# Performance work log

Hardware: AMD Instinct MI355X
Metric: run time of the kernel (lower is better)

## Reference

```python
import jax, jax.numpy as jnp
import numpy as np

IN_FEATS = 512
OUT_FEATS = 512
N = 8192
M = 8192


def setup_inputs() -> dict:
    key = jax.random.key(0)
    k1, k2, k3 = jax.random.split(key, 3)
    feat_p = jax.random.normal(k1, (N, IN_FEATS), dtype=jnp.float32)
    feat_s = jax.random.normal(k2, (M, IN_FEATS), dtype=jnp.float32)
    # He (kaiming uniform) init: bound = sqrt(6 / fan_in)
    bound = float(np.sqrt(6.0 / IN_FEATS))
    weight_a = jax.random.uniform(k3, (IN_FEATS, OUT_FEATS), dtype=jnp.float32,
                                  minval=-bound, maxval=bound)
    return {"feat_p": feat_p, "feat_s": feat_s, "weight_a": weight_a}


def reference(feat_p, feat_s, weight_a):
    h_i = feat_p @ weight_a            # [N, out]
    h_j = feat_s @ weight_a            # [M, out]
    a_ij = jax.nn.relu(h_i @ h_j.T)    # [N, M]
    fro = jnp.sqrt(jnp.sum(a_ij * a_ij))
    alpha = a_ij / fro                 # global Frobenius-norm normalization
    c_i = alpha @ feat_s               # [N, in]
    return c_i
```

## Files before the change

kernel.cpp:

```cpp
#include <hip/hip_runtime.h>
#include <hip/hip_bf16.h>

#define NROWS 8192
#define DIM   512

typedef short v8s __attribute__((ext_vector_type(8)));
typedef short v4s __attribute__((ext_vector_type(4)));
typedef float v4f __attribute__((ext_vector_type(4)));

#define ASM_VMCNT(n) asm volatile("s_waitcnt vmcnt(" #n ")" ::: "memory")
#define ASM_LGKM0    asm volatile("s_waitcnt lgkmcnt(0)" ::: "memory")
#define BAR          __builtin_amdgcn_s_barrier()

__device__ __forceinline__ short f2bf(float f) {
    union { float f; unsigned u; } v; v.f = f;
    unsigned r = (v.u + 0x7fffu + ((v.u >> 16) & 1u)) >> 16;
    return (short)r;
}

__device__ __forceinline__ void stage16(const void* g, void* l) {
    typedef __attribute__((address_space(1))) const unsigned GA;
    typedef __attribute__((address_space(3))) unsigned LA;
    __builtin_amdgcn_global_load_lds((GA*)(const unsigned*)g, (LA*)(unsigned*)l, 16, 0, 0);
}

__global__ __launch_bounds__(256) void transpose_cast_kernel(
        const float* __restrict__ in, short* __restrict__ out, int R, int C) {
    __shared__ float t[32][33];
    const int lx = threadIdx.x & 31;
    const int ly = threadIdx.x >> 5;
    const int r0 = blockIdx.x * 32;
    const int c0 = blockIdx.y * 32;
#pragma unroll
    for (int p = 0; p < 4; ++p)
        t[ly + 8 * p][lx] = in[(size_t)(r0 + ly + 8 * p) * C + c0 + lx];
    __syncthreads();
#pragma unroll
    for (int p = 0; p < 4; ++p)
        out[(size_t)(c0 + ly + 8 * p) * R + r0 + lx] = f2bf(t[lx][ly + 8 * p]);
}

__global__ __launch_bounds__(256) void gemm1_kernel(
        const float* __restrict__ F, const short* __restrict__ WT,
        short* __restrict__ H) {
    const int lane = threadIdx.x & 63;
    const int wid  = threadIdx.x >> 6;
    const int lr = lane & 15, lg = lane >> 4;
    const int r0 = blockIdx.x * 64 + wid * 16;
    const int c0 = blockIdx.y * 64;

    v4f acc[4] = {};
#pragma unroll
    for (int kc = 0; kc < 16; ++kc) {
        const int k = kc * 32 + lg * 8;
        const float* ap = F + (size_t)(r0 + lr) * DIM + k;
        float4 f0 = *(const float4*)ap;
        float4 f1 = *(const float4*)(ap + 4);
        v8s a;
        a[0] = f2bf(f0.x); a[1] = f2bf(f0.y); a[2] = f2bf(f0.z); a[3] = f2bf(f0.w);
        a[4] = f2bf(f1.x); a[5] = f2bf(f1.y); a[6] = f2bf(f1.z); a[7] = f2bf(f1.w);
#pragma unroll
        for (int ct = 0; ct < 4; ++ct) {
            v8s b = *(const v8s*)(WT + (size_t)(c0 + ct * 16 + lr) * DIM + k);
            acc[ct] = __builtin_amdgcn_mfma_f32_16x16x32_bf16(a, b, acc[ct], 0, 0, 0);
        }
    }
#pragma unroll
    for (int ct = 0; ct < 4; ++ct)
#pragma unroll
        for (int i = 0; i < 4; ++i)
            H[(size_t)(r0 + lg * 4 + i) * DIM + c0 + ct * 16 + lr] = f2bf(acc[ct][i]);
}

#define JSPLIT 4
#define JT_PER_BLOCK (NROWS / 64 / JSPLIT)

__device__ __forceinline__ void stage_chunk(const short* __restrict__ Hs,
        short* buf, int j0, int cchunk, int wid, int lane) {
#pragma unroll
    for (int s = 0; s < 2; ++s) {
        const int L = ((wid * 2 + s) * 64 + lane) * 16;
        const int row = L >> 8;
        const int p = L & 255;
        const int c = p ^ ((row & 7) << 4);
        const char* g = (const char*)Hs + ((size_t)(j0 + row) << 10) + (cchunk << 8) + c;
        stage16(g, (char*)buf + L);
    }
}

__device__ __forceinline__ void compute_chunk(const short* buf, const v8s* afrag,
        int cchunk, int half, int lr, int lg, v4f& s0, v4f& s1) {
    const int xo = (lr & 7) << 4;
#pragma unroll
    for (int kc = 0; kc < 4; ++kc) {
        const int col = kc * 64 + lg * 16;
        const int r0 = half * 32 + lr;
        v8s hb0 = *(const v8s*)((const char*)buf + r0 * 256 + (col ^ xo));
        v8s hb1 = *(const v8s*)((const char*)buf + (r0 + 16) * 256 + (col ^ xo));
        s0 = __builtin_amdgcn_mfma_f32_16x16x32_bf16(afrag[cchunk * 4 + kc], hb0, s0, 0, 0, 0);
        s1 = __builtin_amdgcn_mfma_f32_16x16x32_bf16(afrag[cchunk * 4 + kc], hb1, s1, 0, 0, 0);
    }
}

__global__ __launch_bounds__(512, 2) void fused_kernel(
        const short* __restrict__ Hp, const short* __restrict__ Hs,
        const short* __restrict__ FsT, float* __restrict__ Cacc,
        float* __restrict__ ssq) {
    __shared__ __align__(16) short HsL[4][64][128];
    __shared__ __align__(16) short Sb[64][72];

    const int lane = threadIdx.x & 63;
    const int wid  = threadIdx.x >> 6;
    const int lr = lane & 15, lg = lane >> 4;

    const int nwg = gridDim.x * gridDim.y;
    const int bid = blockIdx.x + gridDim.x * blockIdx.y;
    const int cpx = nwg >> 3;
    const int swz = (bid & 7) * cpx + (bid >> 3);
    const int bx = swz % gridDim.x;
    const int by = swz / gridDim.x;

    const int m0    = bx * 64;
    const int strip = wid >> 1;
    const int half  = wid & 1;

    v8s afrag[16];
#pragma unroll
    for (int kc = 0; kc < 16; ++kc)
        afrag[kc] = *(const v8s*)(Hp + (size_t)(m0 + strip * 16 + lr) * DIM + kc * 32 + lg * 8);

    v4f accC[16] = {};
    float ssq_l = 0.f;

    const int jt0 = by * JT_PER_BLOCK;
#pragma unroll
    for (int cc = 0; cc < 4; ++cc)
        stage_chunk(Hs, &HsL[cc][0][0], jt0 * 64, cc, wid, lane);
    ASM_VMCNT(0);

    for (int jt = jt0; jt < jt0 + JT_PER_BLOCK; ++jt) {
        const int j = jt * 64;
        BAR;

        v8s bF[8];
#pragma unroll
        for (int ct = 0; ct < 4; ++ct)
#pragma unroll
            for (int kc2 = 0; kc2 < 2; ++kc2)
                bF[ct * 2 + kc2] = *(const v8s*)(FsT +
                    (size_t)(wid * 64 + ct * 16 + lr) * NROWS + j + kc2 * 32 + lg * 8);

        v4f s0 = {}, s1 = {};
        __builtin_amdgcn_s_setprio(1);
        compute_chunk(&HsL[0][0][0], afrag, 0, half, lr, lg, s0, s1);
        compute_chunk(&HsL[1][0][0], afrag, 1, half, lr, lg, s0, s1);
        compute_chunk(&HsL[2][0][0], afrag, 2, half, lr, lg, s0, s1);
        compute_chunk(&HsL[3][0][0], afrag, 3, half, lr, lg, s0, s1);
        __builtin_amdgcn_s_setprio(0);

#pragma unroll
        for (int i = 0; i < 4; ++i) {
            float v0 = fmaxf(s0[i], 0.f), v1 = fmaxf(s1[i], 0.f);
            ssq_l += v0 * v0 + v1 * v1;
            const int r = strip * 16 + lg * 4 + i;
            Sb[r][(half * 2 + 0) * 16 + lr] = f2bf(v0);
            Sb[r][(half * 2 + 1) * 16 + lr] = f2bf(v1);
        }
        ASM_LGKM0; BAR;

        const int jn = (jt + 1 < jt0 + JT_PER_BLOCK) ? (jt + 1) * 64 : jt0 * 64;
#pragma unroll
        for (int cc = 0; cc < 4; ++cc)
            stage_chunk(Hs, &HsL[cc][0][0], jn, cc, wid, lane);

        ASM_VMCNT(8);

        __builtin_amdgcn_s_setprio(1);
#pragma unroll
        for (int kc2 = 0; kc2 < 2; ++kc2)
#pragma unroll
            for (int mt = 0; mt < 4; ++mt) {
                v8s aS = *(const v8s*)&Sb[mt * 16 + lr][kc2 * 32 + lg * 8];
#pragma unroll
                for (int ct = 0; ct < 4; ++ct)
                    accC[mt * 4 + ct] = __builtin_amdgcn_mfma_f32_16x16x32_bf16(
                        aS, bF[ct * 2 + kc2], accC[mt * 4 + ct], 0, 0, 0);
            }
        __builtin_amdgcn_s_setprio(0);

        ASM_VMCNT(0);
    }

    float w = ssq_l;
#pragma unroll
    for (int off = 32; off; off >>= 1) w += __shfl_down(w, off);
    if (lane == 0) atomicAdd(ssq, w);

#pragma unroll
    for (int mt = 0; mt < 4; ++mt)
#pragma unroll
        for (int ct = 0; ct < 4; ++ct)
#pragma unroll
            for (int i = 0; i < 4; ++i)
                atomicAdd(&Cacc[(size_t)(m0 + mt * 16 + lg * 4 + i) * DIM +
                                wid * 64 + ct * 16 + lr],
                          accC[mt * 4 + ct][i]);
}

__global__ __launch_bounds__(256) void scale_kernel(float* __restrict__ C,
                                                    const float* __restrict__ ssq) {
    const float rs = 1.0f / sqrtf(*ssq);
    const size_t i = (size_t)blockIdx.x * blockDim.x + threadIdx.x;
    float4* p = (float4*)C;
    float4 v = p[i];
    v.x *= rs; v.y *= rs; v.z *= rs; v.w *= rs;
    p[i] = v;
}

extern "C" void kernel_launch(void* const* d_in, const int* in_sizes, int n_in,
                              void* d_out, int out_size, void* d_ws, size_t ws_size,
                              hipStream_t stream) {
    const float* feat_p   = (const float*)d_in[0];
    const float* feat_s   = (const float*)d_in[1];
    const float* weight_a = (const float*)d_in[2];

    char* ws = (char*)d_ws;
    float* ssqp = (float*)ws;
    short* WT   = (short*)(ws + 512);
    short* Hp   = (short*)(ws + 512 + 524288);
    short* Hs   = (short*)(ws + 512 + 524288 + 8388608);
    short* FsT  = (short*)(ws + 512 + 524288 + 16777216);

    transpose_cast_kernel<<<dim3(DIM / 32, DIM / 32), 256, 0, stream>>>(weight_a, WT, DIM, DIM);
    transpose_cast_kernel<<<dim3(NROWS / 32, DIM / 32), 256, 0, stream>>>(feat_s, FsT, NROWS, DIM);

    gemm1_kernel<<<dim3(NROWS / 64, DIM / 64), 256, 0, stream>>>(feat_p, WT, Hp);
    gemm1_kernel<<<dim3(NROWS / 64, DIM / 64), 256, 0, stream>>>(feat_s, WT, Hs);

    hipMemsetAsync(d_out, 0, (size_t)out_size * sizeof(float), stream);
    hipMemsetAsync(ssqp, 0, sizeof(float), stream);

    fused_kernel<<<dim3(NROWS / 64, JSPLIT), 512, 0, stream>>>(Hp, Hs, FsT, (float*)d_out, ssqp);

    scale_kernel<<<(out_size / 4 + 255) / 256, 256, 0, stream>>>((float*)d_out, ssqp);
}
```

Measured before the change: 417.1 us.

## Software-pipeline fused kernel with double-buffered Hs tiles and S buffers

Restructures the fused attention kernel so the second GEMM (S·Fs) for tile t-1 runs in the same iteration as the first GEMM for tile t. Hs is staged whole per tile into a two-slot LDS ring, and the S buffer is double-buffered, which leaves one barrier per iteration instead of two. Each wave now computes a 32x16 S block over the full K, holding two A fragments, so register pressure rises. The two gemm1 launches are also merged into one grid using a z dimension. LDS use roughly doubles, which may limit occupancy at two blocks per CU.

```diff
diff --git a/kernel.cpp b/kernel.cpp
--- a/kernel.cpp
+++ b/kernel.cpp
@@ -5,11 +5,11 @@
 #define DIM   512
 
 typedef short v8s __attribute__((ext_vector_type(8)));
-typedef short v4s __attribute__((ext_vector_type(4)));
 typedef float v4f __attribute__((ext_vector_type(4)));
 
 #define ASM_VMCNT(n) asm volatile("s_waitcnt vmcnt(" #n ")" ::: "memory")
 #define ASM_LGKM0    asm volatile("s_waitcnt lgkmcnt(0)" ::: "memory")
+#define ASM_FENCE    asm volatile("" ::: "memory")
 #define BAR          __builtin_amdgcn_s_barrier()
 
 __device__ __forceinline__ short f2bf(float f) {
@@ -41,8 +41,11 @@
 }
 
 __global__ __launch_bounds__(256) void gemm1_kernel(
-        const float* __restrict__ F, const short* __restrict__ WT,
-        short* __restrict__ H) {
+        const float* __restrict__ Fp, const float* __restrict__ Fs,
+        const short* __restrict__ WT,
+        short* __restrict__ Hp, short* __restrict__ Hs) {
+    const float* F = blockIdx.z ? Fs : Fp;
+    short* H = blockIdx.z ? Hs : Hp;
     const int lane = threadIdx.x & 63;
     const int wid  = threadIdx.x >> 6;
     const int lr = lane & 15, lg = lane >> 4;
@@ -75,43 +78,46 @@
 #define JSPLIT 4
 #define JT_PER_BLOCK (NROWS / 64 / JSPLIT)
 
-__device__ __forceinline__ void stage_chunk(const short* __restrict__ Hs,
-        short* buf, int j0, int cchunk, int wid, int lane) {
-#pragma unroll
-    for (int s = 0; s < 2; ++s) {
-        const int L = ((wid * 2 + s) * 64 + lane) * 16;
-        const int row = L >> 8;
-        const int p = L & 255;
-        const int c = p ^ ((row & 7) << 4);
-        const char* g = (const char*)Hs + ((size_t)(j0 + row) << 10) + (cchunk << 8) + c;
-        stage16(g, (char*)buf + L);
-    }
-}
-
-__device__ __forceinline__ void compute_chunk(const short* buf, const v8s* afrag,
-        int cchunk, int half, int lr, int lg, v4f& s0, v4f& s1) {
-    const int xo = (lr & 7) << 4;
-#pragma unroll
-    for (int kc = 0; kc < 4; ++kc) {
-        const int col = kc * 64 + lg * 16;
-        const int r0 = half * 32 + lr;
-        v8s hb0 = *(const v8s*)((const char*)buf + r0 * 256 + (col ^ xo));
-        v8s hb1 = *(const v8s*)((const char*)buf + (r0 + 16) * 256 + (col ^ xo));
-        s0 = __builtin_amdgcn_mfma_f32_16x16x32_bf16(afrag[cchunk * 4 + kc], hb0, s0, 0, 0, 0);
-        s1 = __builtin_amdgcn_mfma_f32_16x16x32_bf16(afrag[cchunk * 4 + kc], hb1, s1, 0, 0, 0);
-    }
+__device__ __forceinline__ void stage_full(const char* __restrict__ HsB,
+        char* ringW, int j0, int tid) {
+#pragma unroll
+    for (int s = 0; s < 8; ++s) {
+        const int L = s * 8192 + tid * 16;
+        const int row = L >> 10;
+        const int c = (L & 1023) ^ ((row & 7) << 4);
+        stage16(HsB + ((size_t)(j0 + row) << 10) + c, ringW + L);
+    }
+}
+
+__device__ __forceinline__ void phase_b(const short (*SbR)[72], const v8s* bF,
+        v4f (&accC)[16], int lr, int lg) {
+    __builtin_amdgcn_s_setprio(1);
+#pragma unroll
+    for (int kc2 = 0; kc2 < 2; ++kc2)
+#pragma unroll
+        for (int mt = 0; mt < 4; ++mt) {
+            v8s aS = *(const v8s*)&SbR[mt * 16 + lr][kc2 * 32 + lg * 8];
+#pragma unroll
+            for (int ct = 0; ct < 4; ++ct)
+                accC[mt * 4 + ct] = __builtin_amdgcn_mfma_f32_16x16x32_bf16(
+                    aS, bF[ct * 2 + kc2], accC[mt * 4 + ct], 0, 0, 0);
+        }
+    __builtin_amdgcn_s_setprio(0);
 }
 
 __global__ __launch_bounds__(512, 2) void fused_kernel(
         const short* __restrict__ Hp, const short* __restrict__ Hs,
         const short* __restrict__ FsT, float* __restrict__ Cacc,
         float* __restrict__ ssq) {
-    __shared__ __align__(16) short HsL[4][64][128];
-    __shared__ __align__(16) short Sb[64][72];
-
-    const int lane = threadIdx.x & 63;
-    const int wid  = threadIdx.x >> 6;
+    __shared__ __align__(16) short HsL[2][64][512];
+    __shared__ __align__(16) short Sb[2][64][72];
+
+    const int tid  = threadIdx.x;
+    const int lane = tid & 63;
+    const int wid  = tid >> 6;
     const int lr = lane & 15, lg = lane >> 4;
+    const int ws = wid >> 2;
+    const int jq = wid & 3;
 
     const int nwg = gridDim.x * gridDim.y;
     const int bid = blockIdx.x + gridDim.x * blockIdx.y;
@@ -120,75 +126,91 @@
     const int bx = swz % gridDim.x;
     const int by = swz / gridDim.x;
 
-    const int m0    = bx * 64;
-    const int strip = wid >> 1;
-    const int half  = wid & 1;
-
-    v8s afrag[16];
-#pragma unroll
-    for (int kc = 0; kc < 16; ++kc)
-        afrag[kc] = *(const v8s*)(Hp + (size_t)(m0 + strip * 16 + lr) * DIM + kc * 32 + lg * 8);
+    const int m0  = bx * 64;
+    const int jt0 = by * JT_PER_BLOCK;
+
+    v8s afrag[2][16];
+#pragma unroll
+    for (int a = 0; a < 2; ++a)
+#pragma unroll
+        for (int kk = 0; kk < 16; ++kk)
+            afrag[a][kk] = *(const v8s*)(Hp +
+                (size_t)(m0 + ws * 32 + a * 16 + lr) * DIM + kk * 32 + lg * 8);
 
     v4f accC[16] = {};
     float ssq_l = 0.f;
 
-    const int jt0 = by * JT_PER_BLOCK;
-#pragma unroll
-    for (int cc = 0; cc < 4; ++cc)
-        stage_chunk(Hs, &HsL[cc][0][0], jt0 * 64, cc, wid, lane);
+    stage_full((const char*)Hs, (char*)&HsL[0][0][0], jt0 * 64, tid);
     ASM_VMCNT(0);
 
-    for (int jt = jt0; jt < jt0 + JT_PER_BLOCK; ++jt) {
-        const int j = jt * 64;
+    auto body = [&](int t, bool doB) {
+        const int jcur  = (jt0 + t) * 64;
+        const int jnext = (t + 1 < JT_PER_BLOCK) ? jcur + 64 : jt0 * 64;
+        short* ringR = &HsL[t & 1][0][0];
+        char*  ringW = (char*)&HsL[(t + 1) & 1][0][0];
+        short (*SbW)[72] = Sb[t & 1];
+        const short (*SbR)[72] = Sb[(t & 1) ^ 1];
+
         BAR;
 
         v8s bF[8];
-#pragma unroll
-        for (int ct = 0; ct < 4; ++ct)
-#pragma unroll
-            for (int kc2 = 0; kc2 < 2; ++kc2)
-                bF[ct * 2 + kc2] = *(const v8s*)(FsT +
-                    (size_t)(wid * 64 + ct * 16 + lr) * NROWS + j + kc2 * 32 + lg * 8);
+        if (doB) {
+            const int jprev = jcur - 64;
+#pragma unroll
+            for (int ct = 0; ct < 4; ++ct)
+#pragma unroll
+                for (int kc2 = 0; kc2 < 2; ++kc2)
+                    bF[ct * 2 + kc2] = *(const v8s*)(FsT +
+                        (size_t)(wid * 64 + ct * 16 + lr) * NROWS + jprev + kc2 * 32 + lg * 8);
+        }
+        ASM_FENCE;
+        stage_full((const char*)Hs, ringW, jnext, tid);
+
+        if (doB) {
+            ASM_VMCNT(8);
+            phase_b(SbR, bF, accC, lr, lg);
+        }
 
         v4f s0 = {}, s1 = {};
+        const char* rowp = (const char*)ringR + (size_t)(jq * 16 + lr) * 1024;
+        const int xo = (lr & 7) << 4;
         __builtin_amdgcn_s_setprio(1);
-        compute_chunk(&HsL[0][0][0], afrag, 0, half, lr, lg, s0, s1);
-        compute_chunk(&HsL[1][0][0], afrag, 1, half, lr, lg, s0, s1);
-        compute_chunk(&HsL[2][0][0], afrag, 2, half, lr, lg, s0, s1);
-        compute_chunk(&HsL[3][0][0], afrag, 3, half, lr, lg, s0, s1);
+#pragma unroll
+        for (int kk = 0; kk < 16; ++kk) {
+            v8s hb = *(const v8s*)(rowp + ((kk * 64 + lg * 16) ^ xo));
+            s0 = __builtin_amdgcn_mfma_f32_16x16x32_bf16(afrag[0][kk], hb, s0, 0, 0, 0);
+            s1 = __builtin_amdgcn_mfma_f32_16x16x32_bf16(afrag[1][kk], hb, s1, 0, 0, 0);
+        }
         __builtin_amdgcn_s_setprio(0);
 
 #pragma unroll
         for (int i = 0; i < 4; ++i) {
             float v0 = fmaxf(s0[i], 0.f), v1 = fmaxf(s1[i], 0.f);
             ssq_l += v0 * v0 + v1 * v1;
-            const int r = strip * 16 + lg * 4 + i;
-            Sb[r][(half * 2 + 0) * 16 + lr] = f2bf(v0);
-            Sb[r][(half * 2 + 1) * 16 + lr] = f2bf(v1);
-        }
-        ASM_LGKM0; BAR;
-
-        const int jn = (jt + 1 < jt0 + JT_PER_BLOCK) ? (jt + 1) * 64 : jt0 * 64;
-#pragma unroll
-        for (int cc = 0; cc < 4; ++cc)
-            stage_chunk(Hs, &HsL[cc][0][0], jn, cc, wid, lane);
-
-        ASM_VMCNT(8);
-
-        __builtin_amdgcn_s_setprio(1);
-#pragma unroll
-        for (int kc2 = 0; kc2 < 2; ++kc2)
-#pragma unroll
-            for (int mt = 0; mt < 4; ++mt) {
-                v8s aS = *(const v8s*)&Sb[mt * 16 + lr][kc2 * 32 + lg * 8];
-#pragma unroll
-                for (int ct = 0; ct < 4; ++ct)
-                    accC[mt * 4 + ct] = __builtin_amdgcn_mfma_f32_16x16x32_bf16(
-                        aS, bF[ct * 2 + kc2], accC[mt * 4 + ct], 0, 0, 0);
-            }
-        __builtin_amdgcn_s_setprio(0);
-
+            SbW[ws * 32 + lg * 4 + i][jq * 16 + lr]      = f2bf(v0);
+            SbW[ws * 32 + 16 + lg * 4 + i][jq * 16 + lr] = f2bf(v1);
+        }
+        ASM_LGKM0;
         ASM_VMCNT(0);
+    };
+
+    for (int tp = 0; tp < JT_PER_BLOCK / 2; ++tp) {
+        body(2 * tp, tp != 0);
+        body(2 * tp + 1, true);
+    }
+
+    BAR;
+    {
+        const int jprev = (jt0 + JT_PER_BLOCK - 1) * 64;
+        v8s bF[8];
+#pragma unroll
+        for (int ct = 0; ct < 4; ++ct)
+#pragma unroll
+            for (int kc2 = 0; kc2 < 2; ++kc2)
+                bF[ct * 2 + kc2] = *(const v8s*)(FsT +
+                    (size_t)(wid * 64 + ct * 16 + lr) * NROWS + jprev + kc2 * 32 + lg * 8);
+        ASM_VMCNT(0);
+        phase_b(Sb[1], bF, accC, lr, lg);
     }
 
     float w = ssq_l;
@@ -234,8 +256,8 @@
     transpose_cast_kernel<<<dim3(DIM / 32, DIM / 32), 256, 0, stream>>>(weight_a, WT, DIM, DIM);
     transpose_cast_kernel<<<dim3(NROWS / 32, DIM / 32), 256, 0, stream>>>(feat_s, FsT, NROWS, DIM);
 
-    gemm1_kernel<<<dim3(NROWS / 64, DIM / 64), 256, 0, stream>>>(feat_p, WT, Hp);
-    gemm1_kernel<<<dim3(NROWS / 64, DIM / 64), 256, 0, stream>>>(feat_s, WT, Hs);
+    gemm1_kernel<<<dim3(NROWS / 64, DIM / 64, 2), 256, 0, stream>>>(
+        feat_p, feat_s, WT, Hp, Hs);
 
     hipMemsetAsync(d_out, 0, (size_t)out_size * sizeof(float), stream);
     hipMemsetAsync(ssqp, 0, sizeof(float), stream);
```

After: 575.0 us. 37.8% more time.
